# Optimization experiments

Hardware: AMD Instinct MI355X
Metric: run time of the kernel (lower is better)

## Reference

```python
import jax, jax.numpy as jnp
import numpy as np

N_NODES = 100000
N_EDGES = 1600000
IN_DIM = 128
OUT_DIM = 128


def setup_inputs() -> dict:
    key = jax.random.key(0)
    k1, k2, k3, k4 = jax.random.split(key, 4)
    x = jax.random.normal(k1, (N_NODES, IN_DIM), dtype=jnp.float32)
    edge_index = jax.random.randint(k2, (2, N_EDGES), 0, N_NODES, dtype=jnp.int64)
    # glorot-ish linear weight, bias, and PReLU per-channel slope (torch default 0.25)
    W = jax.random.normal(k3, (IN_DIM, OUT_DIM), dtype=jnp.float32) * (1.0 / np.sqrt(IN_DIM))
    b = jax.random.normal(k4, (OUT_DIM,), dtype=jnp.float32) * 0.01
    alpha = jnp.full((OUT_DIM,), 0.25, dtype=jnp.float32)
    return {"x": x, "edge_index": edge_index, "W": W, "b": b, "alpha": alpha}


def reference(x, edge_index, W, b, alpha):
    N = x.shape[0]
    # add self loops (GCNConv default add_self_loops=True)
    loop = jnp.arange(N, dtype=edge_index.dtype)
    src = jnp.concatenate([edge_index[0], loop])  # [E+N]
    dst = jnp.concatenate([edge_index[1], loop])
    # symmetric normalization: deg computed at targets (includes self loops)
    ones = jnp.ones(dst.shape[0], dtype=x.dtype)
    deg = jax.ops.segment_sum(ones, dst, num_segments=N)  # [N]
    dinv = jnp.where(deg > 0, jax.lax.rsqrt(deg), 0.0)
    norm = dinv[src] * dinv[dst]  # [E+N]
    # dense linear transform, then gather-normalize-scatter aggregation
    h = x @ W  # [N, OUT_DIM]
    msg = h[src] * norm[:, None]  # [E+N, OUT_DIM]
    agg = jax.ops.segment_sum(msg, dst, num_segments=N) + b  # [N, OUT_DIM]
    # PReLU with per-channel slope
    z = jnp.where(agg > 0, agg, alpha * agg)
    return z
```

## Files before the change

kernel.cpp:

```cpp
#include <hip/hip_runtime.h>
#include <hip/hip_bf16.h>
#include <cstdint>

#define DIM 128
#define BK_SHIFT 7
#define BK_NODES 128
#define MAX_BUCKETS 1024
#define CUR_STRIDE 16
#define ST 4096
#define EPT 16
#define CAP 2560
#define WPB 64

typedef float f32x4  __attribute__((ext_vector_type(4)));
typedef short bf16x8 __attribute__((ext_vector_type(8)));

__device__ __forceinline__ unsigned bf16_rne(float f) {
    unsigned u = __float_as_uint(f);
    return (u + 0x7fffu + ((u >> 16) & 1u)) >> 16;
}

__global__ __launch_bounds__(256) void init_kernel(const float* __restrict__ x,
                                                   ushort* __restrict__ y,
                                                   const float* __restrict__ W,
                                                   ushort* __restrict__ Wt,
                                                   int* __restrict__ bcursor,
                                                   int N, int pb, int wb, int nbk) {
    int b = blockIdx.x, tid = threadIdx.x;
    if (b < pb) {
        int t = b * 256 + tid;
        if (t < N * (DIM / 4)) {
            float4 v = ((const float4*)x)[t];
            uint2 o;
            o.x = bf16_rne(v.x) | (bf16_rne(v.y) << 16);
            o.y = bf16_rne(v.z) | (bf16_rne(v.w) << 16);
            ((uint2*)y)[t] = o;
        }
    } else if (b < pb + wb) {
        int idx = (b - pb) * 256 + tid;
        if (idx < DIM * DIM) {
            int k = idx >> 7, c = idx & (DIM - 1);
            Wt[c * DIM + k] = (ushort)bf16_rne(W[idx]);
        }
    } else {
        int idx = (b - pb - wb) * 256 + tid;
        if (idx < nbk * CUR_STRIDE) bcursor[idx] = 0;
    }
}

__global__ __launch_bounds__(256) void scatter_kernel(const int* __restrict__ src,
                                                      const int* __restrict__ dst,
                                                      int* __restrict__ bcursor,
                                                      int* __restrict__ bbuf,
                                                      int E, int nbk) {
    __shared__ int h[MAX_BUCKETS];
    for (int i = threadIdx.x; i < nbk; i += 256) h[i] = 0;
    __syncthreads();
    int base = blockIdx.x * ST;
    int bk[EPT], rk[EPT], pk[EPT];
    #pragma unroll
    for (int k = 0; k < EPT; ++k) {
        int e = base + k * 256 + threadIdx.x;
        bk[k] = -1;
        if (e < E) {
            int d = dst[e];
            int b = ((unsigned)d) >> BK_SHIFT;
            bk[k] = b;
            pk[k] = (src[e] << BK_SHIFT) | (d & (BK_NODES - 1));
            rk[k] = atomicAdd(&h[b], 1);
        }
    }
    __syncthreads();
    for (int i = threadIdx.x; i < nbk; i += 256) {
        int c = h[i];
        h[i] = c ? atomicAdd(&bcursor[i * CUR_STRIDE], c) : 0;
    }
    __syncthreads();
    #pragma unroll
    for (int k = 0; k < EPT; ++k) {
        if (bk[k] >= 0) {
            int pos = h[bk[k]] + rk[k];
            if (pos < CAP) bbuf[(size_t)bk[k] * CAP + pos] = pk[k];
        }
    }
}

__global__ __launch_bounds__(256) void build_csr_kernel(const int* __restrict__ bbuf,
                                                        const int* __restrict__ bcursor,
                                                        int* __restrict__ obeg,
                                                        int* __restrict__ oend,
                                                        float* __restrict__ dinv,
                                                        int* __restrict__ csr_src,
                                                        int N) {
    __shared__ int cnt[BK_NODES];
    __shared__ int sc[BK_NODES];
    __shared__ int cur[BK_NODES];
    int b = blockIdx.x, tid = threadIdx.x;
    int count = bcursor[b * CUR_STRIDE];
    if (count > CAP) count = CAP;
    int base = b * CAP;
    if (tid < BK_NODES) cnt[tid] = 0;
    __syncthreads();
    for (int j = tid; j < count; j += 256)
        atomicAdd(&cnt[bbuf[base + j] & (BK_NODES - 1)], 1);
    __syncthreads();
    if (tid < BK_NODES) sc[tid] = cnt[tid];
    __syncthreads();
    for (int d = 1; d < BK_NODES; d <<= 1) {
        int v = (tid >= d && tid < BK_NODES) ? sc[tid - d] : 0;
        __syncthreads();
        if (tid < BK_NODES) sc[tid] += v;
        __syncthreads();
    }
    if (tid < BK_NODES) {
        int node = b * BK_NODES + tid;
        int start = base + sc[tid] - cnt[tid];
        cur[tid] = start;
        if (node < N) {
            obeg[node] = start;
            oend[node] = start + cnt[tid];
            dinv[node] = rsqrtf((float)(cnt[tid] + 1));
        }
    }
    __syncthreads();
    for (int j = tid; j < count; j += 256) {
        int p = bbuf[base + j];
        int pos = atomicAdd(&cur[p & (BK_NODES - 1)], 1);
        csr_src[pos] = p >> BK_SHIFT;
    }
}

__device__ __forceinline__ void agg_accum(float* a, uint4 v, float wt) {
    a[0] += wt * __uint_as_float(v.x << 16);
    a[1] += wt * __uint_as_float(v.x & 0xffff0000u);
    a[2] += wt * __uint_as_float(v.y << 16);
    a[3] += wt * __uint_as_float(v.y & 0xffff0000u);
    a[4] += wt * __uint_as_float(v.z << 16);
    a[5] += wt * __uint_as_float(v.z & 0xffff0000u);
    a[6] += wt * __uint_as_float(v.w << 16);
    a[7] += wt * __uint_as_float(v.w & 0xffff0000u);
}

__global__ __launch_bounds__(1024) void agg_gemm_kernel(const ushort* __restrict__ y,
                                                        const int* __restrict__ csr_src,
                                                        const int* __restrict__ obeg,
                                                        const int* __restrict__ oend,
                                                        const float* __restrict__ dinv,
                                                        const ushort* __restrict__ Wt,
                                                        const float* __restrict__ bias,
                                                        const float* __restrict__ alpha,
                                                        float* __restrict__ out, int N) {
    __shared__ ushort hT[WPB][136];
    __shared__ int nodectr;
    int tid  = threadIdx.x;
    int lane = tid & 63;
    int g = lane >> 4;
    int m = lane & 15;
    if (tid == 0) nodectr = 0;
    __syncthreads();

    for (;;) {
        int local;
        if (lane == 0) local = atomicAdd(&nodectr, 1);
        local = __builtin_amdgcn_readfirstlane(local);
        if (local >= WPB) break;
        int node = blockIdx.x * WPB + local;

        float a[8];
        #pragma unroll
        for (int c = 0; c < 8; ++c) a[c] = 0.f;
        float di = 0.f;

        if (node < N) {
            int beg = obeg[node];
            int cnt = oend[node] - beg;
            di = dinv[node];

            {
                uint4 v = ((const uint4*)(y + (size_t)node * DIM))[m];
                agg_accum(a, v, (g == 0) ? di : 0.f);
            }

            int t = g;
            int nit = (cnt + 7) >> 3;
            for (int it = 0; it < nit; ++it, t += 8) {
                int tB = t + 4;
                int iA = beg + (t  < cnt ? t  : cnt - 1);
                int iB = beg + (tB < cnt ? tB : cnt - 1);
                int sA = csr_src[iA];
                int sB = csr_src[iB];
                float wA = (t  < cnt) ? dinv[sA] : 0.f;
                float wB = (tB < cnt) ? dinv[sB] : 0.f;
                uint4 vA = ((const uint4*)(y + (size_t)sA * DIM))[m];
                uint4 vB = ((const uint4*)(y + (size_t)sB * DIM))[m];
                agg_accum(a, vA, wA);
                agg_accum(a, vB, wB);
            }

            #pragma unroll
            for (int c = 0; c < 8; ++c) {
                a[c] += __shfl_xor(a[c], 16);
                a[c] += __shfl_xor(a[c], 32);
            }
        }

        if (g == 0) {
            uint4 o;
            o.x = bf16_rne(di * a[0]) | (bf16_rne(di * a[1]) << 16);
            o.y = bf16_rne(di * a[2]) | (bf16_rne(di * a[3]) << 16);
            o.z = bf16_rne(di * a[4]) | (bf16_rne(di * a[5]) << 16);
            o.w = bf16_rne(di * a[6]) | (bf16_rne(di * a[7]) << 16);
            *(uint4*)(&hT[local][m * 8]) = o;
        }
    }
    __syncthreads();

    int wid = __builtin_amdgcn_readfirstlane((int)(tid >> 6));
    int r = lane & 15, quad = lane >> 4;
    for (int task = wid; task < 32; task += 16) {
        int rt = task >> 3, ct = task & 7;
        f32x4 acc = (f32x4){0.f, 0.f, 0.f, 0.f};
        #pragma unroll
        for (int ks = 0; ks < 4; ++ks) {
            bf16x8 av = *(const bf16x8*)(&hT[rt * 16 + r][ks * 32 + quad * 8]);
            bf16x8 bv = *(const bf16x8*)(Wt + (size_t)(ct * 16 + r) * DIM + ks * 32 + quad * 8);
            acc = __builtin_amdgcn_mfma_f32_16x16x32_bf16(av, bv, acc, 0, 0, 0);
        }
        int col = ct * 16 + r;
        float bb = bias[col], al = alpha[col];
        int rowbase = blockIdx.x * WPB + rt * 16;
        #pragma unroll
        for (int reg = 0; reg < 4; ++reg) {
            int grow = rowbase + quad * 4 + reg;
            if (grow < N) {
                float vv = acc[reg] + bb;
                vv = vv > 0.f ? vv : al * vv;
                out[(size_t)grow * DIM + col] = vv;
            }
        }
    }
}

extern "C" void kernel_launch(void* const* d_in, const int* in_sizes, int n_in,
                              void* d_out, int out_size, void* d_ws, size_t ws_size,
                              hipStream_t stream) {
    const float* x     = (const float*)d_in[0];
    const int*   ei    = (const int*)d_in[1];
    const float* W     = (const float*)d_in[2];
    const float* bias  = (const float*)d_in[3];
    const float* alpha = (const float*)d_in[4];
    float* out = (float*)d_out;

    int N = in_sizes[0] / DIM;
    int E = in_sizes[1] / 2;
    const int* src = ei;
    const int* dst = ei + E;
    int nbk = (N + BK_NODES - 1) >> BK_SHIFT;

    char* ws = (char*)d_ws;
    size_t off = 0;
    auto alloc = [&](size_t bytes) -> char* {
        char* p = ws + off;
        off += (bytes + 255) & ~(size_t)255;
        return p;
    };
    int*    bbuf    = (int*)alloc((size_t)nbk * CAP * 4);
    int*    csr_src = (int*)alloc((size_t)nbk * CAP * 4);
    ushort* y       = (ushort*)alloc((size_t)N * DIM * 2);
    int*    bcursor = (int*)alloc((size_t)nbk * CUR_STRIDE * 4);
    int*    obeg    = (int*)alloc((size_t)N * 4);
    int*    oend    = (int*)alloc((size_t)N * 4);
    float*  dinv    = (float*)alloc((size_t)N * 4);
    ushort* Wt      = (ushort*)alloc((size_t)DIM * DIM * 2);

    int pb = (N * (DIM / 4) + 255) / 256;
    int wb = (DIM * DIM + 255) / 256;
    int zb = (nbk * CUR_STRIDE + 255) / 256;

    init_kernel<<<pb + wb + zb, 256, 0, stream>>>(x, y, W, Wt, bcursor, N, pb, wb, nbk);
    scatter_kernel<<<(E + ST - 1) / ST, 256, 0, stream>>>(src, dst, bcursor, bbuf, E, nbk);
    build_csr_kernel<<<nbk, 256, 0, stream>>>(bbuf, bcursor, obeg, oend, dinv, csr_src, N);
    agg_gemm_kernel<<<(N + WPB - 1) / WPB, 1024, 0, stream>>>(y, csr_src, obeg, oend, dinv,
                                                              Wt, bias, alpha, out, N);
}
```

Baseline: 241.6 us.

## Make aggregation-GEMM kernel persistent with atomic tile queue and register-cached weights

The aggregation+GEMM kernel becomes persistent: 512 blocks take 64-node tiles from a global atomic counter rather than one block per tile. Each wave now loads its slice of the bf16 weight into registers once, instead of reloading it from global memory for every tile. The scatter kernel is also reshaped to 1024-thread blocks handling 16384 edges each, which cuts the number of blocks and per-bucket global atomics. The persistent loop adds two block barriers per tile and a global atomic. Fewer scatter blocks means less parallelism during the bucketing phase.

```diff
diff --git a/kernel.cpp b/kernel.cpp
--- a/kernel.cpp
+++ b/kernel.cpp
@@ -7,10 +7,11 @@
 #define BK_NODES 128
 #define MAX_BUCKETS 1024
 #define CUR_STRIDE 16
-#define ST 4096
+#define ST 16384
 #define EPT 16
 #define CAP 2560
 #define WPB 64
+#define PERSIST_BLOCKS 512
 
 typedef float f32x4  __attribute__((ext_vector_type(4)));
 typedef short bf16x8 __attribute__((ext_vector_type(8)));
@@ -44,23 +45,23 @@
         }
     } else {
         int idx = (b - pb - wb) * 256 + tid;
-        if (idx < nbk * CUR_STRIDE) bcursor[idx] = 0;
-    }
-}
-
-__global__ __launch_bounds__(256) void scatter_kernel(const int* __restrict__ src,
-                                                      const int* __restrict__ dst,
-                                                      int* __restrict__ bcursor,
-                                                      int* __restrict__ bbuf,
-                                                      int E, int nbk) {
+        if (idx < nbk * CUR_STRIDE + 16) bcursor[idx] = 0;
+    }
+}
+
+__global__ __launch_bounds__(1024) void scatter_kernel(const int* __restrict__ src,
+                                                       const int* __restrict__ dst,
+                                                       int* __restrict__ bcursor,
+                                                       int* __restrict__ bbuf,
+                                                       int E, int nbk) {
     __shared__ int h[MAX_BUCKETS];
-    for (int i = threadIdx.x; i < nbk; i += 256) h[i] = 0;
+    for (int i = threadIdx.x; i < nbk; i += 1024) h[i] = 0;
     __syncthreads();
     int base = blockIdx.x * ST;
     int bk[EPT], rk[EPT], pk[EPT];
     #pragma unroll
     for (int k = 0; k < EPT; ++k) {
-        int e = base + k * 256 + threadIdx.x;
+        int e = base + k * 1024 + threadIdx.x;
         bk[k] = -1;
         if (e < E) {
             int d = dst[e];
@@ -71,7 +72,7 @@
         }
     }
     __syncthreads();
-    for (int i = threadIdx.x; i < nbk; i += 256) {
+    for (int i = threadIdx.x; i < nbk; i += 1024) {
         int c = h[i];
         h[i] = c ? atomicAdd(&bcursor[i * CUR_STRIDE], c) : 0;
     }
@@ -149,93 +150,108 @@
                                                         const ushort* __restrict__ Wt,
                                                         const float* __restrict__ bias,
                                                         const float* __restrict__ alpha,
-                                                        float* __restrict__ out, int N) {
+                                                        float* __restrict__ out,
+                                                        int* __restrict__ gctr,
+                                                        int N, int ntiles) {
     __shared__ ushort hT[WPB][136];
-    __shared__ int nodectr;
+    __shared__ int s_tile, nodectr;
     int tid  = threadIdx.x;
     int lane = tid & 63;
+    int wid  = __builtin_amdgcn_readfirstlane((int)(tid >> 6));
     int g = lane >> 4;
     int m = lane & 15;
-    if (tid == 0) nodectr = 0;
-    __syncthreads();
+
+    int ct  = wid & 7;
+    int rt0 = wid >> 3;
+    bf16x8 bfrag[4];
+    #pragma unroll
+    for (int ks = 0; ks < 4; ++ks)
+        bfrag[ks] = *(const bf16x8*)(Wt + (size_t)(ct * 16 + m) * DIM + ks * 32 + g * 8);
+    int col = ct * 16 + m;
+    float bb = bias[col], al = alpha[col];
 
     for (;;) {
-        int local;
-        if (lane == 0) local = atomicAdd(&nodectr, 1);
-        local = __builtin_amdgcn_readfirstlane(local);
-        if (local >= WPB) break;
-        int node = blockIdx.x * WPB + local;
-
-        float a[8];
+        __syncthreads();
+        if (tid == 0) { s_tile = atomicAdd(gctr, 1); nodectr = 0; }
+        __syncthreads();
+        int tile = s_tile;
+        if (tile >= ntiles) break;
+        int nbase = tile * WPB;
+
+        for (;;) {
+            int local;
+            if (lane == 0) local = atomicAdd(&nodectr, 1);
+            local = __builtin_amdgcn_readfirstlane(local);
+            if (local >= WPB) break;
+            int node = nbase + local;
+
+            float a[8];
+            #pragma unroll
+            for (int c = 0; c < 8; ++c) a[c] = 0.f;
+            float di = 0.f;
+
+            if (node < N) {
+                int beg = obeg[node];
+                int cnt = oend[node] - beg;
+                di = dinv[node];
+
+                {
+                    uint4 v = ((const uint4*)(y + (size_t)node * DIM))[m];
+                    agg_accum(a, v, (g == 0) ? di : 0.f);
+                }
+
+                int t = g;
+                int nit = (cnt + 7) >> 3;
+                for (int it = 0; it < nit; ++it, t += 8) {
+                    int tB = t + 4;
+                    int iA = beg + (t  < cnt ? t  : cnt - 1);
+                    int iB = beg + (tB < cnt ? tB : cnt - 1);
+                    int sA = csr_src[iA];
+                    int sB = csr_src[iB];
+                    float wA = (t  < cnt) ? dinv[sA] : 0.f;
+                    float wB = (tB < cnt) ? dinv[sB] : 0.f;
+                    uint4 vA = ((const uint4*)(y + (size_t)sA * DIM))[m];
+                    uint4 vB = ((const uint4*)(y + (size_t)sB * DIM))[m];
+                    agg_accum(a, vA, wA);
+                    agg_accum(a, vB, wB);
+                }
+
+                #pragma unroll
+                for (int c = 0; c < 8; ++c) {
+                    a[c] += __shfl_xor(a[c], 16);
+                    a[c] += __shfl_xor(a[c], 32);
+                }
+            }
+
+            if (g == 0) {
+                uint4 o;
+                o.x = bf16_rne(di * a[0]) | (bf16_rne(di * a[1]) << 16);
+                o.y = bf16_rne(di * a[2]) | (bf16_rne(di * a[3]) << 16);
+                o.z = bf16_rne(di * a[4]) | (bf16_rne(di * a[5]) << 16);
+                o.w = bf16_rne(di * a[6]) | (bf16_rne(di * a[7]) << 16);
+                *(uint4*)(&hT[local][m * 8]) = o;
+            }
+        }
+        __syncthreads();
+
         #pragma unroll
-        for (int c = 0; c < 8; ++c) a[c] = 0.f;
-        float di = 0.f;
-
-        if (node < N) {
-            int beg = obeg[node];
-            int cnt = oend[node] - beg;
-            di = dinv[node];
-
-            {
-                uint4 v = ((const uint4*)(y + (size_t)node * DIM))[m];
-                agg_accum(a, v, (g == 0) ? di : 0.f);
+        for (int tt = 0; tt < 2; ++tt) {
+            int rt = rt0 + tt * 2;
+            f32x4 acc = (f32x4){0.f, 0.f, 0.f, 0.f};
+            #pragma unroll
+            for (int ks = 0; ks < 4; ++ks) {
+                bf16x8 av = *(const bf16x8*)(&hT[rt * 16 + m][ks * 32 + g * 8]);
+                acc = __builtin_amdgcn_mfma_f32_16x16x32_bf16(av, bfrag[ks], acc, 0, 0, 0);
             }
-
-            int t = g;
-            int nit = (cnt + 7) >> 3;
-            for (int it = 0; it < nit; ++it, t += 8) {
-                int tB = t + 4;
-                int iA = beg + (t  < cnt ? t  : cnt - 1);
-                int iB = beg + (tB < cnt ? tB : cnt - 1);
-                int sA = csr_src[iA];
-                int sB = csr_src[iB];
-                float wA = (t  < cnt) ? dinv[sA] : 0.f;
-                float wB = (tB < cnt) ? dinv[sB] : 0.f;
-                uint4 vA = ((const uint4*)(y + (size_t)sA * DIM))[m];
-                uint4 vB = ((const uint4*)(y + (size_t)sB * DIM))[m];
-                agg_accum(a, vA, wA);
-                agg_accum(a, vB, wB);
-            }
-
+            int rowbase = nbase + rt * 16;
             #pragma unroll
-            for (int c = 0; c < 8; ++c) {
-                a[c] += __shfl_xor(a[c], 16);
-                a[c] += __shfl_xor(a[c], 32);
-            }
-        }
-
-        if (g == 0) {
-            uint4 o;
-            o.x = bf16_rne(di * a[0]) | (bf16_rne(di * a[1]) << 16);
-            o.y = bf16_rne(di * a[2]) | (bf16_rne(di * a[3]) << 16);
-            o.z = bf16_rne(di * a[4]) | (bf16_rne(di * a[5]) << 16);
-            o.w = bf16_rne(di * a[6]) | (bf16_rne(di * a[7]) << 16);
-            *(uint4*)(&hT[local][m * 8]) = o;
-        }
-    }
-    __syncthreads();
-
-    int wid = __builtin_amdgcn_readfirstlane((int)(tid >> 6));
-    int r = lane & 15, quad = lane >> 4;
-    for (int task = wid; task < 32; task += 16) {
-        int rt = task >> 3, ct = task & 7;
-        f32x4 acc = (f32x4){0.f, 0.f, 0.f, 0.f};
-        #pragma unroll
-        for (int ks = 0; ks < 4; ++ks) {
-            bf16x8 av = *(const bf16x8*)(&hT[rt * 16 + r][ks * 32 + quad * 8]);
-            bf16x8 bv = *(const bf16x8*)(Wt + (size_t)(ct * 16 + r) * DIM + ks * 32 + quad * 8);
-            acc = __builtin_amdgcn_mfma_f32_16x16x32_bf16(av, bv, acc, 0, 0, 0);
-        }
-        int col = ct * 16 + r;
-        float bb = bias[col], al = alpha[col];
-        int rowbase = blockIdx.x * WPB + rt * 16;
-        #pragma unroll
-        for (int reg = 0; reg < 4; ++reg) {
-            int grow = rowbase + quad * 4 + reg;
-            if (grow < N) {
-                float vv = acc[reg] + bb;
-                vv = vv > 0.f ? vv : al * vv;
-                out[(size_t)grow * DIM + col] = vv;
+            for (int reg = 0; reg < 4; ++reg) {
+                int grow = rowbase + g * 4 + reg;
+                if (grow < N) {
+                    float vv = acc[reg] + bb;
+                    vv = vv > 0.f ? vv : al * vv;
+                    out[(size_t)grow * DIM + col] = vv;
+                }
             }
         }
     }
@@ -256,6 +272,7 @@
     const int* src = ei;
     const int* dst = ei + E;
     int nbk = (N + BK_NODES - 1) >> BK_SHIFT;
+    int ntiles = (N + WPB - 1) / WPB;
 
     char* ws = (char*)d_ws;
     size_t off = 0;
@@ -267,19 +284,20 @@
     int*    bbuf    = (int*)alloc((size_t)nbk * CAP * 4);
     int*    csr_src = (int*)alloc((size_t)nbk * CAP * 4);
     ushort* y       = (ushort*)alloc((size_t)N * DIM * 2);
-    int*    bcursor = (int*)alloc((size_t)nbk * CUR_STRIDE * 4);
+    int*    bcursor = (int*)alloc(((size_t)nbk * CUR_STRIDE + 16) * 4);
     int*    obeg    = (int*)alloc((size_t)N * 4);
     int*    oend    = (int*)alloc((size_t)N * 4);
     float*  dinv    = (float*)alloc((size_t)N * 4);
     ushort* Wt      = (ushort*)alloc((size_t)DIM * DIM * 2);
+    int*    gctr    = bcursor + (size_t)nbk * CUR_STRIDE;
 
     int pb = (N * (DIM / 4) + 255) / 256;
     int wb = (DIM * DIM + 255) / 256;
-    int zb = (nbk * CUR_STRIDE + 255) / 256;
+    int zb = (nbk * CUR_STRIDE + 16 + 255) / 256;
 
     init_kernel<<<pb + wb + zb, 256, 0, stream>>>(x, y, W, Wt, bcursor, N, pb, wb, nbk);
-    scatter_kernel<<<(E + ST - 1) / ST, 256, 0, stream>>>(src, dst, bcursor, bbuf, E, nbk);
+    scatter_kernel<<<(E + ST - 1) / ST, 1024, 0, stream>>>(src, dst, bcursor, bbuf, E, nbk);
     build_csr_kernel<<<nbk, 256, 0, stream>>>(bbuf, bcursor, obeg, oend, dinv, csr_src, N);
-    agg_gemm_kernel<<<(N + WPB - 1) / WPB, 1024, 0, stream>>>(y, csr_src, obeg, oend, dinv,
-                                                              Wt, bias, alpha, out, N);
-}
+    agg_gemm_kernel<<<PERSIST_BLOCKS, 1024, 0, stream>>>(y, csr_src, obeg, oend, dinv,
+                                                         Wt, bias, alpha, out, gctr, N, ntiles);
+}
```

After: 228.0 us. 1.06x faster.
